# Optimization experiments

Hardware: AMD Instinct MI355X
Metric: run time of the kernel (lower is better)

Reference implementation:

```python
import jax, jax.numpy as jnp
import numpy as np
import math

NUM_HEADS = 8
D_HEAD = 128
DEPTH = 1
LAMBDA_INIT = 0.8 - 0.6 * math.exp(-0.3 * DEPTH)
EPS = 1e-5


def setup_inputs() -> dict:
    key = jax.random.key(0)
    ks = jax.random.split(key, 10)
    B, N, D = 2, 2048, 1024
    s = 0.02
    return {
        "X": jax.random.normal(ks[0], (B, N, D), jnp.float32),
        "Wq": jax.random.normal(ks[1], (2 * D_HEAD * NUM_HEADS, D), jnp.float32) * s,
        "Wk": jax.random.normal(ks[2], (2 * D_HEAD * NUM_HEADS, D), jnp.float32) * s,
        "Wv": jax.random.normal(ks[3], (2 * D_HEAD * NUM_HEADS, D), jnp.float32) * s,
        "Wo": jax.random.normal(ks[4], (D, 2 * D_HEAD * NUM_HEADS), jnp.float32) * s,
        "lambda_q1": jax.random.normal(ks[5], (NUM_HEADS, D_HEAD), jnp.float32) * 0.1,
        "lambda_k1": jax.random.normal(ks[6], (NUM_HEADS, D_HEAD), jnp.float32) * 0.1,
        "lambda_q2": jax.random.normal(ks[7], (NUM_HEADS, D_HEAD), jnp.float32) * 0.1,
        "lambda_k2": jax.random.normal(ks[8], (NUM_HEADS, D_HEAD), jnp.float32) * 0.1,
        "rms_scale": jnp.ones((2 * D_HEAD,), jnp.float32),
    }


def reference(X, Wq, Wk, Wv, Wo, lambda_q1, lambda_k1, lambda_q2, lambda_k2, rms_scale):
    B, N, D = X.shape
    H, dh = NUM_HEADS, D_HEAD

    def proj(W):
        # (B, N, 2*H*dh) -> (B, H, N, 2*dh)
        y = jnp.einsum('bnd,ed->bne', X, W)
        return y.reshape(B, N, H, 2 * dh).transpose(0, 2, 1, 3)

    Q = proj(Wq)
    K = proj(Wk)
    V = proj(Wv)
    Q1, Q2 = Q[..., :dh], Q[..., dh:]
    K1, K2 = K[..., :dh], K[..., dh:]

    lam1 = jnp.exp(jnp.sum(lambda_q1 * lambda_k1, axis=-1))  # (H,)
    lam2 = jnp.exp(jnp.sum(lambda_q2 * lambda_k2, axis=-1))
    lam = (lam1 - lam2 + LAMBDA_INIT)[None, :, None, None]  # (1, H, 1, 1)

    scaling = 1.0 / math.sqrt(dh)
    A1 = jnp.einsum('bhqd,bhkd->bhqk', Q1, K1) * scaling
    A2 = jnp.einsum('bhqd,bhkd->bhqk', Q2, K2) * scaling
    attn = jax.nn.softmax(A1, axis=-1) - lam * jax.nn.softmax(A2, axis=-1)

    O = jnp.einsum('bhqk,bhkd->bhqd', attn, V)  # (B, H, N, 2*dh)
    rms = jnp.sqrt(jnp.mean(O * O, axis=-1, keepdims=True) + EPS)
    O = O / rms * rms_scale
    O = O * (1.0 - LAMBDA_INIT)
    O = O.transpose(0, 2, 1, 3).reshape(B, N, H * 2 * dh)
    return jnp.einsum('bne,de->bnd', O, Wo)
```

## Files before the change

### kernel.cpp

```cpp
#include <hip/hip_runtime.h>
#include <hip/hip_bf16.h>

typedef __bf16 bf16;
typedef __attribute__((ext_vector_type(8))) __bf16 bf16x8;
typedef __attribute__((ext_vector_type(4))) float f32x4;

#define LAMBDA_INIT_F 0.3555090675909693f
#define RMS_EPS 1e-5f
#define QSCALE_F 0.1275174053237f

__device__ __forceinline__ void gl_lds16(const bf16* g, bf16* l) {
  __builtin_amdgcn_global_load_lds(
      (const __attribute__((address_space(1))) unsigned int*)g,
      (__attribute__((address_space(3))) unsigned int*)l, 16, 0, 0);
}

__global__ void fused_cast(const float* __restrict__ X, const float* __restrict__ Wq,
                           const float* __restrict__ Wk, const float* __restrict__ Wv,
                           const float* __restrict__ Wo, bf16* __restrict__ out) {
  constexpr int T4 = 3145728;
  int idx = blockIdx.x * blockDim.x + threadIdx.x;
  int stride = gridDim.x * blockDim.x;
  for (int i = idx; i < T4; i += stride) {
    const float* src;
    int off;
    if (i < 1048576)       { src = X;  off = i; }
    else if (i < 1572864)  { src = Wq; off = i - 1048576; }
    else if (i < 2097152)  { src = Wk; off = i - 1572864; }
    else if (i < 2621440)  { src = Wv; off = i - 2097152; }
    else                   { src = Wo; off = i - 2621440; }
    float4 v = reinterpret_cast<const float4*>(src)[off];
    bf16 o[4];
    o[0] = (bf16)v.x; o[1] = (bf16)v.y; o[2] = (bf16)v.z; o[3] = (bf16)v.w;
    *reinterpret_cast<ushort4*>(&out[(size_t)i * 4]) = *reinterpret_cast<const ushort4*>(o);
  }
}

template <int MODE, int BM>
__global__ __launch_bounds__(256) void gemm_bt(
    const bf16* __restrict__ A, const bf16* __restrict__ B,
    void* __restrict__ Cv, int M, int N, int K) {
  constexpr int BN = 128, BK = 32;
  constexpr int MF = BM / 32;
  constexpr int CA = BM / 16;
  __shared__ __align__(16) bf16 As[2][BM * BK];
  __shared__ __align__(16) bf16 Bs[2][BN * BK];
  const int tid = threadIdx.x, lane = tid & 63, w = tid >> 6;
  const int l15 = lane & 15, lhi = lane >> 4;
  const int wr = (w >> 1) * (BM / 2), wc = (w & 1) * 64;
  const int bm = blockIdx.x * BM, bn = blockIdx.y * BN;
  const int srow = lane >> 2, scol = (lane & 3) * 8;
  const int NTK = K / BK;
  f32x4 acc[MF][4] = {};

  auto stage = [&](int buf, int k0) {
#pragma unroll
    for (int i = 0; i < CA / 4; ++i) {
      int c = w * (CA / 4) + i;
      gl_lds16(&A[(size_t)(bm + c * 16 + srow) * K + k0 + scol], &As[buf][c * 512]);
    }
#pragma unroll
    for (int i = 0; i < 2; ++i) {
      int c = w * 2 + i;
      gl_lds16(&B[(size_t)(bn + c * 16 + srow) * K + k0 + scol], &Bs[buf][c * 512]);
    }
  };

  stage(0, 0);
  __syncthreads();
  for (int t = 0; t < NTK; ++t) {
    const int buf = t & 1;
    if (t + 1 < NTK) stage(buf ^ 1, (t + 1) * BK);
    bf16x8 af[MF], bfr[4];
#pragma unroll
    for (int mf = 0; mf < MF; ++mf)
      af[mf] = *reinterpret_cast<const bf16x8*>(&As[buf][(wr + mf * 16 + l15) * BK + lhi * 8]);
#pragma unroll
    for (int nf = 0; nf < 4; ++nf)
      bfr[nf] = *reinterpret_cast<const bf16x8*>(&Bs[buf][(wc + nf * 16 + l15) * BK + lhi * 8]);
#pragma unroll
    for (int mf = 0; mf < MF; ++mf)
#pragma unroll
      for (int nf = 0; nf < 4; ++nf)
        acc[mf][nf] = __builtin_amdgcn_mfma_f32_16x16x32_bf16(af[mf], bfr[nf], acc[mf][nf], 0, 0, 0);
    __syncthreads();
  }

#pragma unroll
  for (int mf = 0; mf < MF; ++mf)
#pragma unroll
    for (int nf = 0; nf < 4; ++nf)
#pragma unroll
      for (int r = 0; r < 4; ++r) {
        int m = bm + wr + mf * 16 + lhi * 4 + r;
        int n = bn + wc + nf * 16 + l15;
        if constexpr (MODE == 1) {
          ((float*)Cv)[(size_t)m * N + n] = acc[mf][nf][r];
        } else {
          int reg = n >> 11, nl = n & 2047;
          if (reg == 0) {
            ((bf16*)Cv)[(size_t)m * 2048 + nl] = (bf16)(acc[mf][nf][r] * QSCALE_F);
          } else if (reg == 1) {
            ((bf16*)Cv)[(size_t)(m + 4096) * 2048 + nl] = (bf16)acc[mf][nf][r];
          } else {
            int bb = m >> 11, nq = m & 2047;
            int hh = nl >> 8, e = nl & 255;
            int k5 = nq & 31;
            int slot = (((k5 >> 2) & 3) << 3) | (((k5 >> 4) & 1) << 2) | (k5 & 3);
            int np = (nq & ~31) | slot;
            ((bf16*)Cv)[(size_t)16777216 + ((((size_t)bb * 8 + hh) * 256 + e) << 11) + np] =
                (bf16)acc[mf][nf][r];
          }
        }
      }
}

__global__ __launch_bounds__(512, 4) void diff_attn(
    const bf16* __restrict__ Q, const bf16* __restrict__ Kb, const bf16* __restrict__ Vtg,
    const float* __restrict__ lq1, const float* __restrict__ lk1,
    const float* __restrict__ lq2, const float* __restrict__ lk2,
    const float* __restrict__ rms_scale, bf16* __restrict__ Ob) {
  constexpr int NSEQ = 2048, E = 2048, KT = 32, NT = NSEQ / KT;
  __shared__ __align__(16) char smem[65536];
  float* Z = (float*)smem;

  const int tid = threadIdx.x, lane = tid & 63, w = tid >> 6;
  const int l15 = lane & 15, lhi = lane >> 4;
  const int g = w >> 1, s = w & 1;

  const int bid = blockIdx.x;
  const int orig = (bid & 7) * 64 + (bid >> 3);
  const int bh = orig >> 5;
  const int qb = orig & 31;
  const int b = bh >> 3, h = bh & 7;
  const int q0 = qb * 64;

  float lam = 0.f;
  if (s) {
    float sl1 = 0.f, sl2 = 0.f;
    for (int i = 0; i < 128; ++i) {
      sl1 += lq1[h * 128 + i] * lk1[h * 128 + i];
      sl2 += lq2[h * 128 + i] * lk2[h * 128 + i];
    }
    lam = __expf(sl1) - __expf(sl2) + LAMBDA_INIT_F;
  }

  const size_t qbase = ((size_t)b * NSEQ + q0 + g * 16 + l15) * E + (size_t)h * 256 + s * 128;
  bf16x8 qf[4];
#pragma unroll
  for (int df = 0; df < 4; ++df)
    qf[df] = *reinterpret_cast<const bf16x8*>(&Q[qbase + df * 32 + lhi * 8]);

  const bf16* Kbase = Kb + ((size_t)b * NSEQ) * E + (size_t)h * 256;
  const bf16* Vbase = Vtg + (((size_t)b * 8 + h) * 256) * (size_t)NSEQ;

  const int krow_sub = lane >> 5;
  const int kslot = lane & 31;
  const int ve_sub = lane >> 2;
  const int vchunk = lane & 3;
  const int swz = l15 & 7;
  const int vq2 = (l15 >> 1) & 3;
  const int voff = (lhi ^ vq2) << 3;

  f32x4 o[16] = {};
  float ll = 0.f;

  auto stage = [&](int buf, int t) {
    const int kt0 = t * KT;
    bf16* Ksl = (bf16*)(smem + buf * 32768);
    bf16* Vsl = Ksl + 8192;
#pragma unroll
    for (int i = 0; i < 2; ++i) {
      int c = w * 2 + i;
      int row = 2 * c + krow_sub;
      gl_lds16(&Kbase[(size_t)(kt0 + row) * E + ((kslot ^ (row & 7)) << 3)], &Ksl[c * 512]);
    }
#pragma unroll
    for (int i = 0; i < 2; ++i) {
      int c = w * 2 + i;
      int e = c * 16 + ve_sub;
      int lc = vchunk ^ ((e >> 1) & 3);
      gl_lds16(&Vbase[(size_t)e * NSEQ + kt0 + (lc << 3)], &Vsl[c * 512]);
    }
  };

  stage(0, 0);
  __syncthreads();

  for (int t = 0; t < NT; ++t) {
    const int buf = t & 1;
    const bf16* Ksl = (const bf16*)(smem + buf * 32768);
    const bf16* Vsl = Ksl + 8192;

    f32x4 sv0 = {}, sv1 = {};
#pragma unroll
    for (int df = 0; df < 4; ++df) {
      const int slot = (((s << 4) + df * 4 + lhi) ^ swz) << 3;
      bf16x8 kf0 = *reinterpret_cast<const bf16x8*>(&Ksl[l15 * 256 + slot]);
      bf16x8 kf1 = *reinterpret_cast<const bf16x8*>(&Ksl[(16 + l15) * 256 + slot]);
      sv0 = __builtin_amdgcn_mfma_f32_16x16x32_bf16(kf0, qf[df], sv0, 0, 0, 0);
      sv1 = __builtin_amdgcn_mfma_f32_16x16x32_bf16(kf1, qf[df], sv1, 0, 0, 0);
    }

    __builtin_amdgcn_sched_barrier(0);
    if (t + 1 < NT) stage(buf ^ 1, t + 1);
    __builtin_amdgcn_sched_barrier(0);

    bf16 pb[8];
    float rsum = 0.f;
#pragma unroll
    for (int r = 0; r < 4; ++r) {
      float e0 = __builtin_amdgcn_exp2f(sv0[r]);
      float e1 = __builtin_amdgcn_exp2f(sv1[r]);
      rsum += e0 + e1;
      pb[r] = (bf16)e0;
      pb[4 + r] = (bf16)e1;
    }
    ll += rsum;
    bf16x8 pa = *reinterpret_cast<const bf16x8*>(pb);

    __builtin_amdgcn_s_setprio(1);
#pragma unroll
    for (int eb = 0; eb < 16; ++eb) {
      bf16x8 vf = *reinterpret_cast<const bf16x8*>(&Vsl[(eb * 16 + l15) * 32 + voff]);
      o[eb] = __builtin_amdgcn_mfma_f32_16x16x32_bf16(pa, vf, o[eb], 0, 0, 0);
    }
    __builtin_amdgcn_s_setprio(0);

    __syncthreads();
  }

  ll += __shfl_xor(ll, 16, 64);
  ll += __shfl_xor(ll, 32, 64);
  float L[4];
#pragma unroll
  for (int r = 0; r < 4; ++r) L[r] = __shfl(ll, 4 * lhi + r, 64);

  if (s) {
    float* Zg = Z + g * 4096;
#pragma unroll
    for (int r = 0; r < 4; ++r) {
      float i2 = lam / L[r];
#pragma unroll
      for (int eb = 0; eb < 16; ++eb)
        Zg[(4 * lhi + r) * 256 + eb * 16 + l15] = o[eb][r] * i2;
    }
  }
  __syncthreads();
  if (!s) {
    const float osc = 1.0f - LAMBDA_INIT_F;
    const float* Zg = Z + g * 4096;
#pragma unroll
    for (int r = 0; r < 4; ++r) {
      float i1 = 1.0f / L[r];
      float vals[16];
      float ssq = 0.f;
#pragma unroll
      for (int eb = 0; eb < 16; ++eb) {
        float v = o[eb][r] * i1 - Zg[(4 * lhi + r) * 256 + eb * 16 + l15];
        vals[eb] = v;
        ssq += v * v;
      }
#pragma unroll
      for (int off = 1; off < 16; off <<= 1) ssq += __shfl_xor(ssq, off, 64);
      float rinv = rsqrtf(ssq * (1.0f / 256.0f) + RMS_EPS);
      const int q = q0 + g * 16 + 4 * lhi + r;
      const size_t ob = ((size_t)b * NSEQ + q) * E + (size_t)h * 256;
#pragma unroll
      for (int eb = 0; eb < 16; ++eb) {
        int e = eb * 16 + l15;
        Ob[ob + e] = (bf16)(vals[eb] * rinv * rms_scale[e] * osc);
      }
    }
  }
}

extern "C" void kernel_launch(void* const* d_in, const int* in_sizes, int n_in,
                              void* d_out, int out_size, void* d_ws, size_t ws_size,
                              hipStream_t stream) {
  const float* X   = (const float*)d_in[0];
  const float* Wq  = (const float*)d_in[1];
  const float* Wk  = (const float*)d_in[2];
  const float* Wv  = (const float*)d_in[3];
  const float* Wo  = (const float*)d_in[4];
  const float* lq1 = (const float*)d_in[5];
  const float* lk1 = (const float*)d_in[6];
  const float* lq2 = (const float*)d_in[7];
  const float* lk2 = (const float*)d_in[8];
  const float* rs  = (const float*)d_in[9];
  float* out = (float*)d_out;

  constexpr size_t B = 2, NSEQ = 2048, D = 1024, E = 2048;
  constexpr size_t M = B * NSEQ;

  char* ws = (char*)d_ws;
  bf16* Xb  = (bf16*)ws;
  bf16* Wqb = Xb + M * D;
  bf16* Wkb = Wqb + E * D;
  bf16* Wvb = Wkb + E * D;
  bf16* Wob = Wvb + E * D;
  bf16* Qb  = Wob + D * E;
  bf16* Kb  = Qb + M * E;
  bf16* Vtb = Kb + M * E;
  bf16* Ob  = Vtb + M * E;

  fused_cast<<<2048, 256, 0, stream>>>(X, Wq, Wk, Wv, Wo, Xb);

  gemm_bt<3, 128><<<dim3(M / 128, 6144 / 128), 256, 0, stream>>>(
      Xb, Wqb, Qb, (int)M, 6144, (int)D);

  diff_attn<<<dim3(512), 512, 0, stream>>>(Qb, Kb, Vtb, lq1, lk1, lq2, lk2, rs, Ob);

  gemm_bt<1, 64><<<dim3(M / 64, D / 128), 256, 0, stream>>>(Ob, Wob, out, (int)M, (int)D, (int)E);
}
```

Before: 238.7 us.

## Double attention query tile, split K/V staging across waves, XCD-aware QKV GEMM tiling

The attention kernel now runs 1024-thread blocks covering 128 queries each, so every K/V tile staged into shared memory serves twice as many queries. Staging is split so half the waves load K and the other half load V. The cross-wave partial output is exchanged through shared memory as bf16 instead of fp32, so the larger block fits the same 64 KB buffer, at some cost in precision. The QKV projection GEMM gets a 1D grid remapped so each XCD works on a contiguous rectangle of tiles, improving L2 reuse of A and B.

New measurement: 250.8 us. +5.1%, slower.

```diff
diff --git a/kernel.cpp b/kernel.cpp
--- a/kernel.cpp
+++ b/kernel.cpp
@@ -48,7 +48,17 @@
   const int tid = threadIdx.x, lane = tid & 63, w = tid >> 6;
   const int l15 = lane & 15, lhi = lane >> 4;
   const int wr = (w >> 1) * (BM / 2), wc = (w & 1) * 64;
-  const int bm = blockIdx.x * BM, bn = blockIdx.y * BN;
+  int bm, bn;
+  if constexpr (MODE == 3) {
+    const int bid = blockIdx.x;
+    const int xcd = bid & 7, t = bid >> 3;
+    const int sx = xcd & 3, sy = xcd >> 2;
+    bn = (sx * 12 + t % 12) * 128;
+    bm = (sy * 16 + t / 12) * 128;
+  } else {
+    bm = blockIdx.x * BM;
+    bn = blockIdx.y * BN;
+  }
   const int srow = lane >> 2, scol = (lane & 3) * 8;
   const int NTK = K / BK;
   f32x4 acc[MF][4] = {};
@@ -115,25 +125,25 @@
       }
 }
 
-__global__ __launch_bounds__(512, 4) void diff_attn(
+__global__ __launch_bounds__(1024, 4) void diff_attn(
     const bf16* __restrict__ Q, const bf16* __restrict__ Kb, const bf16* __restrict__ Vtg,
     const float* __restrict__ lq1, const float* __restrict__ lk1,
     const float* __restrict__ lq2, const float* __restrict__ lk2,
     const float* __restrict__ rms_scale, bf16* __restrict__ Ob) {
   constexpr int NSEQ = 2048, E = 2048, KT = 32, NT = NSEQ / KT;
   __shared__ __align__(16) char smem[65536];
-  float* Z = (float*)smem;
+  bf16* Zb = (bf16*)smem;
 
   const int tid = threadIdx.x, lane = tid & 63, w = tid >> 6;
   const int l15 = lane & 15, lhi = lane >> 4;
   const int g = w >> 1, s = w & 1;
 
   const int bid = blockIdx.x;
-  const int orig = (bid & 7) * 64 + (bid >> 3);
-  const int bh = orig >> 5;
-  const int qb = orig & 31;
+  const int orig = (bid & 7) * 32 + (bid >> 3);
+  const int bh = orig >> 4;
+  const int qb = orig & 15;
   const int b = bh >> 3, h = bh & 7;
-  const int q0 = qb * 64;
+  const int q0 = qb * 128;
 
   float lam = 0.f;
   if (s) {
@@ -169,18 +179,21 @@
     const int kt0 = t * KT;
     bf16* Ksl = (bf16*)(smem + buf * 32768);
     bf16* Vsl = Ksl + 8192;
-#pragma unroll
-    for (int i = 0; i < 2; ++i) {
-      int c = w * 2 + i;
-      int row = 2 * c + krow_sub;
-      gl_lds16(&Kbase[(size_t)(kt0 + row) * E + ((kslot ^ (row & 7)) << 3)], &Ksl[c * 512]);
-    }
-#pragma unroll
-    for (int i = 0; i < 2; ++i) {
-      int c = w * 2 + i;
-      int e = c * 16 + ve_sub;
-      int lc = vchunk ^ ((e >> 1) & 3);
-      gl_lds16(&Vbase[(size_t)e * NSEQ + kt0 + (lc << 3)], &Vsl[c * 512]);
+    if (w < 8) {
+#pragma unroll
+      for (int i = 0; i < 2; ++i) {
+        int c = w * 2 + i;
+        int row = 2 * c + krow_sub;
+        gl_lds16(&Kbase[(size_t)(kt0 + row) * E + ((kslot ^ (row & 7)) << 3)], &Ksl[c * 512]);
+      }
+    } else {
+#pragma unroll
+      for (int i = 0; i < 2; ++i) {
+        int c = (w - 8) * 2 + i;
+        int e = c * 16 + ve_sub;
+        int lc = vchunk ^ ((e >> 1) & 3);
+        gl_lds16(&Vbase[(size_t)e * NSEQ + kt0 + (lc << 3)], &Vsl[c * 512]);
+      }
     }
   };
 
@@ -237,19 +250,19 @@
   for (int r = 0; r < 4; ++r) L[r] = __shfl(ll, 4 * lhi + r, 64);
 
   if (s) {
-    float* Zg = Z + g * 4096;
+    bf16* Zg = Zb + g * 4096;
 #pragma unroll
     for (int r = 0; r < 4; ++r) {
       float i2 = lam / L[r];
 #pragma unroll
       for (int eb = 0; eb < 16; ++eb)
-        Zg[(4 * lhi + r) * 256 + eb * 16 + l15] = o[eb][r] * i2;
+        Zg[(4 * lhi + r) * 256 + eb * 16 + l15] = (bf16)(o[eb][r] * i2);
     }
   }
   __syncthreads();
   if (!s) {
     const float osc = 1.0f - LAMBDA_INIT_F;
-    const float* Zg = Z + g * 4096;
+    const bf16* Zg = Zb + g * 4096;
 #pragma unroll
     for (int r = 0; r < 4; ++r) {
       float i1 = 1.0f / L[r];
@@ -257,7 +270,7 @@
       float ssq = 0.f;
 #pragma unroll
       for (int eb = 0; eb < 16; ++eb) {
-        float v = o[eb][r] * i1 - Zg[(4 * lhi + r) * 256 + eb * 16 + l15];
+        float v = o[eb][r] * i1 - (float)Zg[(4 * lhi + r) * 256 + eb * 16 + l15];
         vals[eb] = v;
         ssq += v * v;
       }
@@ -306,10 +319,9 @@
 
   fused_cast<<<2048, 256, 0, stream>>>(X, Wq, Wk, Wv, Wo, Xb);
 
-  gemm_bt<3, 128><<<dim3(M / 128, 6144 / 128), 256, 0, stream>>>(
-      Xb, Wqb, Qb, (int)M, 6144, (int)D);
-
-  diff_attn<<<dim3(512), 512, 0, stream>>>(Qb, Kb, Vtb, lq1, lk1, lq2, lk2, rs, Ob);
+  gemm_bt<3, 128><<<dim3(1536), 256, 0, stream>>>(Xb, Wqb, Qb, (int)M, 6144, (int)D);
+
+  diff_attn<<<dim3(256), 1024, 0, stream>>>(Qb, Kb, Vtb, lq1, lk1, lq2, lk2, rs, Ob);
 
   gemm_bt<1, 64><<<dim3(M / 64, D / 128), 256, 0, stream>>>(Ob, Wob, out, (int)M, (int)D, (int)E);
 }
```
